# Optimization experiments

Measured on AMD Instinct MI355X. Metric: run time of the kernel, lower is better.

The kernel has to match this reference:

```python
import jax, jax.numpy as jnp
import numpy as np

B, T, C = 4, 4096, 512


def setup_inputs() -> dict:
    key = jax.random.key(0)
    ks = jax.random.split(key, 7)
    s = 1.0 / np.sqrt(C)  # ~ torch Linear init scale
    X = jax.random.normal(ks[0], (B, T, C), jnp.float32)
    S_n = jnp.zeros((B, C, C), jnp.float32)
    W_Q = jax.random.normal(ks[1], (C, C), jnp.float32) * s
    b_Q = jax.random.normal(ks[2], (C,), jnp.float32) * s
    W_K = jax.random.normal(ks[3], (C, C), jnp.float32) * s
    b_K = jax.random.normal(ks[4], (C,), jnp.float32) * s
    W_V = jax.random.normal(ks[5], (C, C), jnp.float32) * s
    b_V = jax.random.normal(ks[6], (C,), jnp.float32) * s
    return {"X": X, "S_n": S_n, "W_Q": W_Q, "b_Q": b_Q,
            "W_K": W_K, "b_K": b_K, "W_V": W_V, "b_V": b_V}


def reference(X, S_n, W_Q, b_Q, W_K, b_K, W_V, b_V):
    # forward_chunkwise with chunk_len = 1 (exact simplification):
    #   per step t (gamma g_t from linspace(0.96, 0.99, T)):
    #     inner_t = (q_t . k_t) * v_t            # D = gamma^0 = 1
    #     cross_t = (q_t @ S) * g_t              # e[:,0,:] = g^1
    #     O_t     = tanh(inner_t + cross_t)
    #     S      <- k_t^T v_t + g_t * S          # D[-1] = 1, g**chunk_len = g
    Bx, Tx, Cx = X.shape
    Q = X @ W_Q + b_Q  # [B,T,C]
    K = X @ W_K + b_K
    V = X @ W_V + b_V
    gammas = jnp.linspace(0.96, 0.99, Tx).astype(X.dtype)

    def step(S, inp):
        q, k, v, g = inp  # q,k,v: [B,C]; g: scalar
        inner = jnp.sum(q * k, axis=-1, keepdims=True) * v      # [B,C]
        cross = jnp.einsum('bc,bcd->bd', q, S) * g              # [B,C]
        O = jnp.tanh(inner + cross)
        S_new = jnp.einsum('bc,bd->bcd', k, v) + S * g          # [B,C,C]
        return S_new, O

    # original resets S_n to zeros regardless of the passed-in value
    S0 = jnp.zeros_like(S_n)
    S_final, O = jax.lax.scan(
        step, S0,
        (Q.transpose(1, 0, 2), K.transpose(1, 0, 2), V.transpose(1, 0, 2), gammas))
    out = O.transpose(1, 0, 2)  # [B,T,C]
    return out, S_final
```

## Files before the change

kernel.cpp:

```cpp
#include <hip/hip_runtime.h>
#include <math.h>

#define Bsz  4
#define Tlen 4096
#define Cdim 512
#define CUT  (-12.0f)
#define NBE  8388608

typedef unsigned int u32;
typedef _Float16 f16;
typedef __attribute__((ext_vector_type(8))) _Float16 f16x8;
typedef __attribute__((ext_vector_type(4))) float floatx4;
#define MFMA_F16(a,b,c) __builtin_amdgcn_mfma_f32_16x16x32_f16((a),(b),(c),0,0,0)

union pun8 { uint4 u; f16x8 f; };

__device__ __forceinline__ u32 pack2(f16 a, f16 b) {
    return (u32)__builtin_bit_cast(unsigned short, a) |
           ((u32)__builtin_bit_cast(unsigned short, b) << 16);
}
__device__ __forceinline__ u32 splitpack(float v) {
    f16 h = (f16)v;
    f16 l = (f16)(v - (float)h);
    return pack2(h, l);
}
__device__ __forceinline__ void unpack8(const u32* p, f16x8& h, f16x8& l) {
    uint4 q0 = *(const uint4*)p;
    uint4 q1 = *(const uint4*)(p + 4);
    pun8 ph, pl;
    ph.u.x = __builtin_amdgcn_perm(q0.y, q0.x, 0x05040100u);
    pl.u.x = __builtin_amdgcn_perm(q0.y, q0.x, 0x07060302u);
    ph.u.y = __builtin_amdgcn_perm(q0.w, q0.z, 0x05040100u);
    pl.u.y = __builtin_amdgcn_perm(q0.w, q0.z, 0x07060302u);
    ph.u.z = __builtin_amdgcn_perm(q1.y, q1.x, 0x05040100u);
    pl.u.z = __builtin_amdgcn_perm(q1.y, q1.x, 0x07060302u);
    ph.u.w = __builtin_amdgcn_perm(q1.w, q1.z, 0x05040100u);
    pl.u.w = __builtin_amdgcn_perm(q1.w, q1.z, 0x07060302u);
    h = ph.f; l = pl.f;
}
__device__ __forceinline__ float tanh_fast(float x) {
    return 1.0f - 2.0f / (__expf(2.0f * x) + 1.0f);
}

__global__ __launch_bounds__(256) void prep_kernel(
    const float* __restrict__ X,
    const float* __restrict__ WQ, const float* __restrict__ WK,
    const float* __restrict__ WV,
    f16* __restrict__ Xf, f16* __restrict__ WT,
    float* __restrict__ Lg, float* __restrict__ Wfin, int* __restrict__ sLo) {
    __shared__ char pshm[18432];
    int bid = blockIdx.x, tid = threadIdx.x;
    if (bid < 2048) {
        size_t i = ((size_t)bid * 256 + tid) * 16;
        float v[16];
#pragma unroll
        for (int j = 0; j < 4; ++j) {
            float4 a = *(const float4*)(X + i + j * 4);
            v[j*4+0]=a.x; v[j*4+1]=a.y; v[j*4+2]=a.z; v[j*4+3]=a.w;
        }
        uint4 o0, o1;
        o0.x = pack2((f16)v[0], (f16)v[1]);   o0.y = pack2((f16)v[2], (f16)v[3]);
        o0.z = pack2((f16)v[4], (f16)v[5]);   o0.w = pack2((f16)v[6], (f16)v[7]);
        o1.x = pack2((f16)v[8], (f16)v[9]);   o1.y = pack2((f16)v[10], (f16)v[11]);
        o1.z = pack2((f16)v[12], (f16)v[13]); o1.w = pack2((f16)v[14], (f16)v[15]);
        *(uint4*)(Xf + i) = o0;
        *(uint4*)(Xf + i + 8) = o1;
    } else if (bid < 2240) {
        f16* tile = (f16*)pshm;
        int wb = bid - 2048;
        int mat = wb >> 6, rem = wb & 63;
        int k0 = (rem >> 3) * 64, n0 = (rem & 7) * 64;
        const float* W = (mat == 0) ? WQ : (mat == 1) ? WK : WV;
        int row = tid >> 2, q = tid & 3;
        const float* src = W + (size_t)(k0 + row) * Cdim + n0 + q * 16;
        float vv[16];
#pragma unroll
        for (int j = 0; j < 4; ++j) {
            float4 v = *(const float4*)(src + j * 4);
            vv[j*4+0]=v.x; vv[j*4+1]=v.y; vv[j*4+2]=v.z; vv[j*4+3]=v.w;
        }
#pragma unroll
        for (int j = 0; j < 16; ++j) tile[(q * 16 + j) * 72 + row] = (f16)vv[j];
        __syncthreads();
        f16x8 r0 = *(const f16x8*)(tile + row * 72 + q * 16);
        f16x8 r1 = *(const f16x8*)(tile + row * 72 + q * 16 + 8);
        f16* dst = WT + ((size_t)mat * Cdim + n0 + row) * Cdim + k0 + q * 16;
        *(f16x8*)dst = r0;
        *(f16x8*)(dst + 8) = r1;
    } else {
        float* Lsh = (float*)pshm;
        float* sums = (float*)(pshm + 16400);
        float lg[16];
        float local = 0.f;
        int base = tid * 16;
#pragma unroll
        for (int i = 0; i < 16; ++i) {
            int t = base + i;
            float g = 0.96f + 0.03f * ((float)t * (1.0f / 4095.0f));
            lg[i] = logf(g);
            local += lg[i];
        }
        sums[tid] = local;
        __syncthreads();
        for (int off = 1; off < 256; off <<= 1) {
            float v = sums[tid];
            if (tid >= off) v += sums[tid - off];
            __syncthreads();
            sums[tid] = v;
            __syncthreads();
        }
        float pre = (tid == 0) ? 0.f : sums[tid - 1];
#pragma unroll
        for (int i = 0; i < 16; ++i) {
            Lsh[base + i] = pre;
            pre += lg[i];
        }
        if (tid == 255) Lsh[4096] = pre;
        __syncthreads();
        for (int t = tid; t < 4097; t += 256) Lg[t] = Lsh[t];
        float LT = Lsh[4096];
        for (int s = tid; s < 4096; s += 256) Wfin[s] = __expf(LT - Lsh[s + 1]);
        if (tid < 128) {
            float ref = Lsh[tid * 32 + 1];
            int st_hi = tid >> 2;
            int lo = st_hi;
            for (int st = 0; st < st_hi; ++st)
                if (ref - Lsh[st * 128 + 128] > CUT) { lo = st; break; }
            sLo[tid] = lo;
        }
    }
}

__global__ __launch_bounds__(256, 2) void qkv_mfma(
    const f16* __restrict__ Xf, const f16* __restrict__ WT,
    const float* __restrict__ bQ, const float* __restrict__ bK,
    const float* __restrict__ bV,
    f16* __restrict__ Qf, f16* __restrict__ Kf,
    f16* __restrict__ KT, f16* __restrict__ VT) {
    __shared__ char smem[34816];
    u32* sX = (u32*)smem;
    u32* sW = (u32*)(smem + 16384);
    f16* sB = (f16*)smem;

    int tid = threadIdx.x, lane = tid & 63, wid = tid >> 6;
    int l16 = lane & 15, quad = lane >> 4;
    int wm = wid & 1, wn = wid >> 1;
    int xb = blockIdx.x;
    int mat = xb >> 2, n0 = (xb & 3) * 128;
    int m0 = blockIdx.y * 128;

    floatx4 acc[4][4];
#pragma unroll
    for (int i = 0; i < 4; ++i)
#pragma unroll
        for (int j = 0; j < 4; ++j) acc[i][j] = (floatx4)0.f;

    int srow = tid >> 1, shalf = tid & 1;
    int arow_a = wm * 64 + l16, arow_b = wn * 64 + l16;
    int swz_f = (l16 & 7) << 2;

    for (int kc = 0; kc < Cdim; kc += 64) {
        __syncthreads();
        {
            const f16* gx = Xf + (size_t)(m0 + srow) * Cdim + kc + shalf * 32;
            const f16* gw = WT + ((size_t)(mat * Cdim) + n0 + srow) * Cdim + kc + shalf * 32;
            int wswz = (srow & 7) << 2;
#pragma unroll
            for (int k = 0; k < 4; ++k) {
                uint4 xv = *(const uint4*)(gx + k * 8);
                uint4 wv = *(const uint4*)(gw + k * 8);
                int w = shalf * 16 + k * 4;
                *(uint4*)&sX[srow * 32 + (w ^ wswz)] = xv;
                *(uint4*)&sW[srow * 32 + (w ^ wswz)] = wv;
            }
        }
        __syncthreads();
#pragma unroll
        for (int ks = 0; ks < 2; ++ks) {
            int w0 = ks * 16 + quad * 4;
            f16x8 af[4], bf[4];
#pragma unroll
            for (int mt = 0; mt < 4; ++mt)
                af[mt] = ((pun8*)&sX[(arow_a + mt * 16) * 32 + (w0 ^ swz_f)])->f;
#pragma unroll
            for (int nt = 0; nt < 4; ++nt)
                bf[nt] = ((pun8*)&sW[(arow_b + nt * 16) * 32 + (w0 ^ swz_f)])->f;
#pragma unroll
            for (int mt = 0; mt < 4; ++mt)
#pragma unroll
                for (int nt = 0; nt < 4; ++nt)
                    acc[mt][nt] = MFMA_F16(af[mt], bf[nt], acc[mt][nt]);
        }
    }

    const float* bias = (mat == 0) ? bQ : (mat == 1) ? bK : bV;
    float bv[4];
#pragma unroll
    for (int nt = 0; nt < 4; ++nt) bv[nt] = bias[n0 + wn * 64 + nt * 16 + l16];
    float cv[4][4][4];
#pragma unroll
    for (int mt = 0; mt < 4; ++mt)
#pragma unroll
        for (int nt = 0; nt < 4; ++nt)
#pragma unroll
            for (int r = 0; r < 4; ++r) cv[mt][nt][r] = acc[mt][nt][r] + bv[nt];

    int b = m0 >> 12, tloc = m0 & 4095;

    if (mat == 2) {
#pragma unroll
        for (int mt = 0; mt < 4; ++mt)
#pragma unroll
            for (int nt = 0; nt < 4; ++nt) {
                int d = n0 + wn * 64 + nt * 16 + l16;
                int t = tloc + wm * 64 + mt * 16 + quad * 4;
                uint2 w;
                w.x = pack2((f16)cv[mt][nt][0], (f16)cv[mt][nt][1]);
                w.y = pack2((f16)cv[mt][nt][2], (f16)cv[mt][nt][3]);
                *(uint2*)(VT + ((size_t)(b * Cdim + d)) * Tlen + t) = w;
            }
    } else {
        if (mat == 1) {
#pragma unroll
            for (int mt = 0; mt < 4; ++mt)
#pragma unroll
                for (int nt = 0; nt < 4; ++nt) {
                    int d = n0 + wn * 64 + nt * 16 + l16;
                    int t = tloc + wm * 64 + mt * 16 + quad * 4;
                    uint2 w;
                    w.x = pack2((f16)cv[mt][nt][0], (f16)cv[mt][nt][1]);
                    w.y = pack2((f16)cv[mt][nt][2], (f16)cv[mt][nt][3]);
                    *(uint2*)(KT + ((size_t)(b * Cdim + d)) * Tlen + t) = w;
                }
        }
        __syncthreads();
#pragma unroll
        for (int mt = 0; mt < 4; ++mt)
#pragma unroll
            for (int nt = 0; nt < 4; ++nt)
#pragma unroll
                for (int r = 0; r < 4; ++r)
                    sB[(wm * 64 + mt * 16 + quad * 4 + r) * 136 +
                       wn * 64 + nt * 16 + l16] = (f16)cv[mt][nt][r];
        __syncthreads();
        {
            f16* Out = (mat == 0) ? Qf : Kf;
            int r2 = tid >> 1, h2 = tid & 1;
            f16* dst = Out + (size_t)(m0 + r2) * Cdim + n0 + h2 * 64;
#pragma unroll
            for (int j = 0; j < 8; ++j)
                *(uint4*)(dst + j * 8) = *(const uint4*)(sB + r2 * 136 + h2 * 64 + j * 8);
        }
    }
}

__global__ __launch_bounds__(512, 4) void attn_mfma(
    const f16* __restrict__ Qf, const f16* __restrict__ Kf,
    const f16* __restrict__ VT, const f16* __restrict__ KT,
    const float* __restrict__ Lg, const float* __restrict__ Wfin,
    const int* __restrict__ sLo, float* __restrict__ out,
    float* __restrict__ S) {
    __shared__ char smem[66560];
    int tid = threadIdx.x, lane = tid & 63, wid = tid >> 6;
    int l16 = lane & 15, quad = lane >> 4;

    if (blockIdx.x >= 512) {
        f16* sA  = (f16*)smem;
        f16* sB2 = (f16*)(smem + 9216);
        int r = blockIdx.x - 512;
        int c0 = (r & 7) * 64, d0 = ((r >> 3) & 7) * 64, bb = r >> 6;
        int wv_c = wid & 3, wv_d = wid >> 2;
        float LT = Lg[Tlen];
        floatx4 acc[2];
        acc[0] = (floatx4)0.f; acc[1] = (floatx4)0.f;
        int s0start = Tlen - 64;
        for (int s0 = 0; s0 < Tlen; s0 += 64)
            if (LT - Lg[s0 + 64] > CUT) { s0start = s0; break; }
        int row = tid >> 3, q8 = (tid & 7) * 8;
        for (int s0 = s0start; s0 < Tlen; s0 += 64) {
            __syncthreads();
            {
                const f16* g = KT + ((size_t)(bb * Cdim + c0 + row)) * Tlen + s0 + q8;
                f16x8 u0 = *(const f16x8*)g;
                float4 w0 = *(const float4*)(Wfin + s0 + q8);
                float4 w1 = *(const float4*)(Wfin + s0 + q8 + 4);
                float wv[8] = {w0.x, w0.y, w0.z, w0.w, w1.x, w1.y, w1.z, w1.w};
                f16x8 o0;
#pragma unroll
                for (int j = 0; j < 8; ++j) o0[j] = (f16)((float)u0[j] * wv[j]);
                *(f16x8*)(sA + row * 72 + q8) = o0;
                const f16* gv = VT + ((size_t)(bb * Cdim + d0 + row)) * Tlen + s0 + q8;
                *(f16x8*)(sB2 + row * 72 + q8) = *(const f16x8*)gv;
            }
            __syncthreads();
#pragma unroll
            for (int ks = 0; ks < 2; ++ks) {
                int ko = ks * 32 + quad * 8;
                f16x8 a0 = *(const f16x8*)(sA + (wv_c * 16 + l16) * 72 + ko);
                f16x8 b0 = *(const f16x8*)(sB2 + (wv_d * 32 + l16) * 72 + ko);
                f16x8 b1 = *(const f16x8*)(sB2 + (wv_d * 32 + 16 + l16) * 72 + ko);
                acc[0] = MFMA_F16(a0, b0, acc[0]);
                acc[1] = MFMA_F16(a0, b1, acc[1]);
            }
        }
#pragma unroll
        for (int dt = 0; dt < 2; ++dt)
#pragma unroll
            for (int rr = 0; rr < 4; ++rr) {
                int c = c0 + wv_c * 16 + quad * 4 + rr;
                int d = d0 + wv_d * 32 + dt * 16 + l16;
                S[((size_t)(bb * Cdim + c)) * Cdim + d] = acc[dt][rr];
            }
        return;
    }

    u32* sQ  = (u32*)smem;
    u32* sPc = (u32*)(smem + 32768);

    int i = blockIdx.x;
    int halfsel = i >> 8, q = i & 255;
    int L = ((q & 7) << 5) | (q >> 3);
    int b = L >> 6, ttl = L & 63;
    int tt = halfsel ? (63 - ttl) : (64 + ttl);
    int t0 = tt * 32;
    size_t bT = (size_t)b * Tlen;
    int lo = sLo[tt], hi = tt >> 2;

    {
        int r = tid >> 4, c16 = tid & 15;
        const f16* src = Qf + (bT + t0 + r) * Cdim + c16 * 32;
        int wswz = (r & 7) << 2;
#pragma unroll
        for (int k = 0; k < 4; ++k) {
            uint4 v = *(const uint4*)(src + k * 8);
            int w = c16 * 16 + k * 4;
            *(uint4*)&sQ[r * 256 + (w ^ wswz)] = v;
        }
    }

    float aT[2][4];
#pragma unroll
    for (int mt = 0; mt < 2; ++mt)
#pragma unroll
        for (int r = 0; r < 4; ++r)
            aT[mt][r] = Lg[t0 + mt * 16 + quad * 4 + r + 1];

    floatx4 oacc[2][4];
#pragma unroll
    for (int mt = 0; mt < 2; ++mt)
#pragma unroll
        for (int nt = 0; nt < 4; ++nt) oacc[mt][nt] = (floatx4)0.f;

    int swz_f = (l16 & 7) << 2;
    int rowA0 = l16 * 256;
    int rowA1 = (16 + l16) * 256;

    __syncthreads();

    int pb = 0;
    for (int st = lo; st <= hi; ++st) {
        int s0 = st * 128;
        float lsp = Lg[s0 + wid * 16 + l16 + 1];

        floatx4 pacc[2];
        pacc[0] = (floatx4)0.f; pacc[1] = (floatx4)0.f;

        const f16* kb = Kf + (bT + s0 + wid * 16 + l16) * Cdim;
        const f16* vb = VT + ((size_t)(b * Cdim + wid * 64 + l16)) * Tlen + s0;

#pragma unroll 4
        for (int kc = 0; kc < 8; ++kc) {
            int ko = kc * 32 + quad * 8;
            int w0 = kc * 16 + quad * 4;
            f16x8 a0 = ((pun8*)&sQ[rowA0 + (w0 ^ swz_f)])->f;
            f16x8 a1 = ((pun8*)&sQ[rowA1 + (w0 ^ swz_f)])->f;
            f16x8 bk = *(const f16x8*)(kb + ko);
            pacc[0] = MFMA_F16(a0, bk, pacc[0]);
            pacc[1] = MFMA_F16(a1, bk, pacc[1]);
        }

        f16x8 vpre[2][4];
#pragma unroll
        for (int kf = 0; kf < 2; ++kf)
#pragma unroll
            for (int nt = 0; nt < 4; ++nt)
                vpre[kf][nt] = *(const f16x8*)(vb + (size_t)nt * 16 * Tlen +
                                               kf * 32 + quad * 8);

#pragma unroll 4
        for (int kc = 8; kc < 16; ++kc) {
            int ko = kc * 32 + quad * 8;
            int w0 = kc * 16 + quad * 4;
            f16x8 a0 = ((pun8*)&sQ[rowA0 + (w0 ^ swz_f)])->f;
            f16x8 a1 = ((pun8*)&sQ[rowA1 + (w0 ^ swz_f)])->f;
            f16x8 bk = *(const f16x8*)(kb + ko);
            pacc[0] = MFMA_F16(a0, bk, pacc[0]);
            pacc[1] = MFMA_F16(a1, bk, pacc[1]);
        }

        u32* sP = sPc + pb * 4224;
#pragma unroll
        for (int mt = 0; mt < 2; ++mt)
#pragma unroll
            for (int r = 0; r < 4; ++r) {
                int tl = mt * 16 + quad * 4 + r;
                int sl = wid * 16 + l16;
                int t = t0 + tl, s = s0 + sl;
                float p = pacc[mt][r];
                p = (s <= t) ? p * __expf(aT[mt][r] - lsp) : 0.f;
                sP[tl * 132 + (sl ^ ((tl & 7) << 4))] = splitpack(p);
            }
        __syncthreads();

        f16x8 vrest[2][4];
#pragma unroll
        for (int kf = 0; kf < 2; ++kf)
#pragma unroll
            for (int nt = 0; nt < 4; ++nt)
                vrest[kf][nt] = *(const f16x8*)(vb + (size_t)nt * 16 * Tlen +
                                                (kf + 2) * 32 + quad * 8);

#pragma unroll
        for (int kf = 0; kf < 4; ++kf) {
            int sb = kf * 32 + quad * 8;
            f16x8 ph[2], pl[2];
#pragma unroll
            for (int mt = 0; mt < 2; ++mt) {
                int tl = mt * 16 + l16;
                unpack8(&sP[tl * 132 + (sb ^ ((tl & 7) << 4))], ph[mt], pl[mt]);
            }
#pragma unroll
            for (int nt = 0; nt < 4; ++nt) {
                f16x8 vf = (kf < 2) ? vpre[kf][nt] : vrest[kf - 2][nt];
#pragma unroll
                for (int mt = 0; mt < 2; ++mt) {
                    oacc[mt][nt] = MFMA_F16(ph[mt], vf, oacc[mt][nt]);
                    oacc[mt][nt] = MFMA_F16(pl[mt], vf, oacc[mt][nt]);
                }
            }
        }
        pb ^= 1;
    }

#pragma unroll
    for (int mt = 0; mt < 2; ++mt)
#pragma unroll
        for (int nt = 0; nt < 4; ++nt)
#pragma unroll
            for (int r = 0; r < 4; ++r) {
                int t = t0 + mt * 16 + quad * 4 + r;
                int d = wid * 64 + nt * 16 + l16;
                out[(bT + t) * (size_t)Cdim + d] = tanh_fast(oacc[mt][nt][r]);
            }
}

extern "C" void kernel_launch(void* const* d_in, const int* in_sizes, int n_in,
                              void* d_out, int out_size, void* d_ws, size_t ws_size,
                              hipStream_t stream) {
    (void)in_sizes; (void)n_in; (void)out_size; (void)ws_size;
    const float* X  = (const float*)d_in[0];
    const float* WQ = (const float*)d_in[2];
    const float* bQ = (const float*)d_in[3];
    const float* WK = (const float*)d_in[4];
    const float* bK = (const float*)d_in[5];
    const float* WV = (const float*)d_in[6];
    const float* bV = (const float*)d_in[7];

    float* out   = (float*)d_out;
    float* S_out = out + (size_t)NBE;

    char* ws = (char*)d_ws;
    f16*   Xf   = (f16*)(ws);
    f16*   Qf   = (f16*)(ws + 2ull * NBE);
    f16*   Kf   = (f16*)(ws + 4ull * NBE);
    f16*   KT   = (f16*)(ws + 6ull * NBE);
    f16*   VT   = (f16*)(ws + 8ull * NBE);
    f16*   WT   = (f16*)(ws + 10ull * NBE);
    char*  tail = ws + 10ull * NBE + (2u << 20);
    float* Lg   = (float*)(tail);
    float* Wfin = (float*)(tail + 16512);
    int*   sLo  = (int*)(tail + 16512 + 16384);

    prep_kernel<<<2241, 256, 0, stream>>>(X, WQ, WK, WV, Xf, WT, Lg, Wfin, sLo);
    qkv_mfma<<<dim3(12, 128), 256, 0, stream>>>(Xf, WT, bQ, bK, bV, Qf, Kf, KT, VT);
    attn_mfma<<<768, 512, 0, stream>>>(Qf, Kf, VT, KT, Lg, Wfin, sLo, out, S_out);
}
```

Baseline: 266.2 us.

## Fuse X conversion into QKV GEMM, widen attention and state tiles

Drops the separate X-to-fp16 pass: the QKV GEMM now loads fp32 X and converts it while staging to shared memory. The attention kernel processes 256-key blocks instead of 128, with one shared P buffer in place of double buffering. The final-state blocks grow to 128x128 tiles, so fewer blocks are launched. The aim is less memory traffic and launch overhead and more reuse per block, at the cost of extra syncs, more registers, and direct global V loads in the second half of each block.

```diff
diff --git a/kernel.cpp b/kernel.cpp
--- a/kernel.cpp
+++ b/kernel.cpp
@@ -43,31 +43,15 @@
 }
 
 __global__ __launch_bounds__(256) void prep_kernel(
-    const float* __restrict__ X,
     const float* __restrict__ WQ, const float* __restrict__ WK,
     const float* __restrict__ WV,
-    f16* __restrict__ Xf, f16* __restrict__ WT,
+    f16* __restrict__ WT,
     float* __restrict__ Lg, float* __restrict__ Wfin, int* __restrict__ sLo) {
     __shared__ char pshm[18432];
     int bid = blockIdx.x, tid = threadIdx.x;
-    if (bid < 2048) {
-        size_t i = ((size_t)bid * 256 + tid) * 16;
-        float v[16];
-#pragma unroll
-        for (int j = 0; j < 4; ++j) {
-            float4 a = *(const float4*)(X + i + j * 4);
-            v[j*4+0]=a.x; v[j*4+1]=a.y; v[j*4+2]=a.z; v[j*4+3]=a.w;
-        }
-        uint4 o0, o1;
-        o0.x = pack2((f16)v[0], (f16)v[1]);   o0.y = pack2((f16)v[2], (f16)v[3]);
-        o0.z = pack2((f16)v[4], (f16)v[5]);   o0.w = pack2((f16)v[6], (f16)v[7]);
-        o1.x = pack2((f16)v[8], (f16)v[9]);   o1.y = pack2((f16)v[10], (f16)v[11]);
-        o1.z = pack2((f16)v[12], (f16)v[13]); o1.w = pack2((f16)v[14], (f16)v[15]);
-        *(uint4*)(Xf + i) = o0;
-        *(uint4*)(Xf + i + 8) = o1;
-    } else if (bid < 2240) {
+    if (bid < 192) {
         f16* tile = (f16*)pshm;
-        int wb = bid - 2048;
+        int wb = bid;
         int mat = wb >> 6, rem = wb & 63;
         int k0 = (rem >> 3) * 64, n0 = (rem & 7) * 64;
         const float* W = (mat == 0) ? WQ : (mat == 1) ? WK : WV;
@@ -122,17 +106,17 @@
         for (int s = tid; s < 4096; s += 256) Wfin[s] = __expf(LT - Lsh[s + 1]);
         if (tid < 128) {
             float ref = Lsh[tid * 32 + 1];
-            int st_hi = tid >> 2;
+            int st_hi = tid >> 3;
             int lo = st_hi;
             for (int st = 0; st < st_hi; ++st)
-                if (ref - Lsh[st * 128 + 128] > CUT) { lo = st; break; }
+                if (ref - Lsh[st * 256 + 256] > CUT) { lo = st; break; }
             sLo[tid] = lo;
         }
     }
 }
 
 __global__ __launch_bounds__(256, 2) void qkv_mfma(
-    const f16* __restrict__ Xf, const f16* __restrict__ WT,
+    const float* __restrict__ X, const f16* __restrict__ WT,
     const float* __restrict__ bQ, const float* __restrict__ bK,
     const float* __restrict__ bV,
     f16* __restrict__ Qf, f16* __restrict__ Kf,
@@ -162,12 +146,18 @@
     for (int kc = 0; kc < Cdim; kc += 64) {
         __syncthreads();
         {
-            const f16* gx = Xf + (size_t)(m0 + srow) * Cdim + kc + shalf * 32;
+            const float* gx = X + (size_t)(m0 + srow) * Cdim + kc + shalf * 32;
             const f16* gw = WT + ((size_t)(mat * Cdim) + n0 + srow) * Cdim + kc + shalf * 32;
             int wswz = (srow & 7) << 2;
 #pragma unroll
             for (int k = 0; k < 4; ++k) {
-                uint4 xv = *(const uint4*)(gx + k * 8);
+                float4 xa = *(const float4*)(gx + k * 8);
+                float4 xc = *(const float4*)(gx + k * 8 + 4);
+                uint4 xv;
+                xv.x = pack2((f16)xa.x, (f16)xa.y);
+                xv.y = pack2((f16)xa.z, (f16)xa.w);
+                xv.z = pack2((f16)xc.x, (f16)xc.y);
+                xv.w = pack2((f16)xc.z, (f16)xc.w);
                 uint4 wv = *(const uint4*)(gw + k * 8);
                 int w = shalf * 16 + k * 4;
                 *(uint4*)&sX[srow * 32 + (w ^ wswz)] = xv;
@@ -260,62 +250,83 @@
     const float* __restrict__ Lg, const float* __restrict__ Wfin,
     const int* __restrict__ sLo, float* __restrict__ out,
     float* __restrict__ S) {
-    __shared__ char smem[66560];
+    __shared__ char smem[66048];
     int tid = threadIdx.x, lane = tid & 63, wid = tid >> 6;
     int l16 = lane & 15, quad = lane >> 4;
 
     if (blockIdx.x >= 512) {
         f16* sA  = (f16*)smem;
-        f16* sB2 = (f16*)(smem + 9216);
+        f16* sB2 = (f16*)(smem + 18432);
         int r = blockIdx.x - 512;
-        int c0 = (r & 7) * 64, d0 = ((r >> 3) & 7) * 64, bb = r >> 6;
-        int wv_c = wid & 3, wv_d = wid >> 2;
+        int c0 = (r & 3) * 128, d0 = ((r >> 2) & 3) * 128, bb = r >> 4;
+        int wv_c = wid & 1, wv_d = wid >> 1;
         float LT = Lg[Tlen];
-        floatx4 acc[2];
-        acc[0] = (floatx4)0.f; acc[1] = (floatx4)0.f;
+        floatx4 acc[4][2];
+#pragma unroll
+        for (int i = 0; i < 4; ++i)
+#pragma unroll
+            for (int jj = 0; jj < 2; ++jj) acc[i][jj] = (floatx4)0.f;
         int s0start = Tlen - 64;
         for (int s0 = 0; s0 < Tlen; s0 += 64)
             if (LT - Lg[s0 + 64] > CUT) { s0start = s0; break; }
-        int row = tid >> 3, q8 = (tid & 7) * 8;
+        int row = tid >> 2, q16 = (tid & 3) * 16;
         for (int s0 = s0start; s0 < Tlen; s0 += 64) {
             __syncthreads();
             {
-                const f16* g = KT + ((size_t)(bb * Cdim + c0 + row)) * Tlen + s0 + q8;
+                const f16* g = KT + ((size_t)(bb * Cdim + c0 + row)) * Tlen + s0 + q16;
                 f16x8 u0 = *(const f16x8*)g;
-                float4 w0 = *(const float4*)(Wfin + s0 + q8);
-                float4 w1 = *(const float4*)(Wfin + s0 + q8 + 4);
-                float wv[8] = {w0.x, w0.y, w0.z, w0.w, w1.x, w1.y, w1.z, w1.w};
-                f16x8 o0;
-#pragma unroll
-                for (int j = 0; j < 8; ++j) o0[j] = (f16)((float)u0[j] * wv[j]);
-                *(f16x8*)(sA + row * 72 + q8) = o0;
-                const f16* gv = VT + ((size_t)(bb * Cdim + d0 + row)) * Tlen + s0 + q8;
-                *(f16x8*)(sB2 + row * 72 + q8) = *(const f16x8*)gv;
+                f16x8 u1 = *(const f16x8*)(g + 8);
+                float wv[16];
+#pragma unroll
+                for (int jj = 0; jj < 4; ++jj) {
+                    float4 w4 = *(const float4*)(Wfin + s0 + q16 + jj * 4);
+                    wv[jj*4+0]=w4.x; wv[jj*4+1]=w4.y; wv[jj*4+2]=w4.z; wv[jj*4+3]=w4.w;
+                }
+                f16x8 o0, o1;
+#pragma unroll
+                for (int jj = 0; jj < 8; ++jj) o0[jj] = (f16)((float)u0[jj] * wv[jj]);
+#pragma unroll
+                for (int jj = 0; jj < 8; ++jj) o1[jj] = (f16)((float)u1[jj] * wv[8 + jj]);
+                *(f16x8*)(sA + row * 72 + q16) = o0;
+                *(f16x8*)(sA + row * 72 + q16 + 8) = o1;
+                const f16* gv = VT + ((size_t)(bb * Cdim + d0 + row)) * Tlen + s0 + q16;
+                uint4 v0 = *(const uint4*)gv, v1 = *(const uint4*)(gv + 8);
+                *(uint4*)(sB2 + row * 72 + q16) = v0;
+                *(uint4*)(sB2 + row * 72 + q16 + 8) = v1;
             }
             __syncthreads();
 #pragma unroll
             for (int ks = 0; ks < 2; ++ks) {
                 int ko = ks * 32 + quad * 8;
-                f16x8 a0 = *(const f16x8*)(sA + (wv_c * 16 + l16) * 72 + ko);
-                f16x8 b0 = *(const f16x8*)(sB2 + (wv_d * 32 + l16) * 72 + ko);
-                f16x8 b1 = *(const f16x8*)(sB2 + (wv_d * 32 + 16 + l16) * 72 + ko);
-                acc[0] = MFMA_F16(a0, b0, acc[0]);
-                acc[1] = MFMA_F16(a0, b1, acc[1]);
-            }
-        }
-#pragma unroll
-        for (int dt = 0; dt < 2; ++dt)
-#pragma unroll
-            for (int rr = 0; rr < 4; ++rr) {
-                int c = c0 + wv_c * 16 + quad * 4 + rr;
-                int d = d0 + wv_d * 32 + dt * 16 + l16;
-                S[((size_t)(bb * Cdim + c)) * Cdim + d] = acc[dt][rr];
-            }
+                f16x8 av[4], bv2[2];
+#pragma unroll
+                for (int ct = 0; ct < 4; ++ct)
+                    av[ct] = *(const f16x8*)(sA + (wv_c * 64 + ct * 16 + l16) * 72 + ko);
+#pragma unroll
+                for (int dt = 0; dt < 2; ++dt)
+                    bv2[dt] = *(const f16x8*)(sB2 + (wv_d * 32 + dt * 16 + l16) * 72 + ko);
+#pragma unroll
+                for (int ct = 0; ct < 4; ++ct)
+#pragma unroll
+                    for (int dt = 0; dt < 2; ++dt)
+                        acc[ct][dt] = MFMA_F16(av[ct], bv2[dt], acc[ct][dt]);
+            }
+        }
+#pragma unroll
+        for (int ct = 0; ct < 4; ++ct)
+#pragma unroll
+            for (int dt = 0; dt < 2; ++dt)
+#pragma unroll
+                for (int rr = 0; rr < 4; ++rr) {
+                    int c = c0 + wv_c * 64 + ct * 16 + quad * 4 + rr;
+                    int d = d0 + wv_d * 32 + dt * 16 + l16;
+                    S[((size_t)(bb * Cdim + c)) * Cdim + d] = acc[ct][dt][rr];
+                }
         return;
     }
 
-    u32* sQ  = (u32*)smem;
-    u32* sPc = (u32*)(smem + 32768);
+    u32* sQ = (u32*)smem;
+    u32* sP = (u32*)(smem + 32768);
 
     int i = blockIdx.x;
     int halfsel = i >> 8, q = i & 255;
@@ -324,7 +335,7 @@
     int tt = halfsel ? (63 - ttl) : (64 + ttl);
     int t0 = tt * 32;
     size_t bT = (size_t)b * Tlen;
-    int lo = sLo[tt], hi = tt >> 2;
+    int lo = sLo[tt], hi = tt >> 3;
 
     {
         int r = tid >> 4, c16 = tid & 15;
@@ -357,15 +368,21 @@
 
     __syncthreads();
 
-    int pb = 0;
     for (int st = lo; st <= hi; ++st) {
-        int s0 = st * 128;
-        float lsp = Lg[s0 + wid * 16 + l16 + 1];
-
-        floatx4 pacc[2];
-        pacc[0] = (floatx4)0.f; pacc[1] = (floatx4)0.f;
-
-        const f16* kb = Kf + (bT + s0 + wid * 16 + l16) * Cdim;
+        int s0 = st * 256;
+        float lsp[2];
+#pragma unroll
+        for (int sq = 0; sq < 2; ++sq)
+            lsp[sq] = Lg[s0 + wid * 32 + sq * 16 + l16 + 1];
+
+        floatx4 pacc[2][2];
+#pragma unroll
+        for (int mt = 0; mt < 2; ++mt)
+#pragma unroll
+            for (int sq = 0; sq < 2; ++sq) pacc[mt][sq] = (floatx4)0.f;
+
+        const f16* kb0 = Kf + (bT + s0 + wid * 32 + l16) * Cdim;
+        const f16* kb1 = kb0 + 16 * Cdim;
         const f16* vb = VT + ((size_t)(b * Cdim + wid * 64 + l16)) * Tlen + s0;
 
 #pragma unroll 4
@@ -374,9 +391,12 @@
             int w0 = kc * 16 + quad * 4;
             f16x8 a0 = ((pun8*)&sQ[rowA0 + (w0 ^ swz_f)])->f;
             f16x8 a1 = ((pun8*)&sQ[rowA1 + (w0 ^ swz_f)])->f;
-            f16x8 bk = *(const f16x8*)(kb + ko);
-            pacc[0] = MFMA_F16(a0, bk, pacc[0]);
-            pacc[1] = MFMA_F16(a1, bk, pacc[1]);
+            f16x8 bk0 = *(const f16x8*)(kb0 + ko);
+            f16x8 bk1 = *(const f16x8*)(kb1 + ko);
+            pacc[0][0] = MFMA_F16(a0, bk0, pacc[0][0]);
+            pacc[0][1] = MFMA_F16(a0, bk1, pacc[0][1]);
+            pacc[1][0] = MFMA_F16(a1, bk0, pacc[1][0]);
+            pacc[1][1] = MFMA_F16(a1, bk1, pacc[1][1]);
         }
 
         f16x8 vpre[2][4];
@@ -393,23 +413,14 @@
             int w0 = kc * 16 + quad * 4;
             f16x8 a0 = ((pun8*)&sQ[rowA0 + (w0 ^ swz_f)])->f;
             f16x8 a1 = ((pun8*)&sQ[rowA1 + (w0 ^ swz_f)])->f;
-            f16x8 bk = *(const f16x8*)(kb + ko);
-            pacc[0] = MFMA_F16(a0, bk, pacc[0]);
-            pacc[1] = MFMA_F16(a1, bk, pacc[1]);
-        }
-
-        u32* sP = sPc + pb * 4224;
-#pragma unroll
-        for (int mt = 0; mt < 2; ++mt)
-#pragma unroll
-            for (int r = 0; r < 4; ++r) {
-                int tl = mt * 16 + quad * 4 + r;
-                int sl = wid * 16 + l16;
-                int t = t0 + tl, s = s0 + sl;
-                float p = pacc[mt][r];
-                p = (s <= t) ? p * __expf(aT[mt][r] - lsp) : 0.f;
-                sP[tl * 132 + (sl ^ ((tl & 7) << 4))] = splitpack(p);
-            }
+            f16x8 bk0 = *(const f16x8*)(kb0 + ko);
+            f16x8 bk1 = *(const f16x8*)(kb1 + ko);
+            pacc[0][0] = MFMA_F16(a0, bk0, pacc[0][0]);
+            pacc[0][1] = MFMA_F16(a0, bk1, pacc[0][1]);
+            pacc[1][0] = MFMA_F16(a1, bk0, pacc[1][0]);
+            pacc[1][1] = MFMA_F16(a1, bk1, pacc[1][1]);
+        }
+
         __syncthreads();
 
         f16x8 vrest[2][4];
@@ -421,17 +432,35 @@
                                                 (kf + 2) * 32 + quad * 8);
 
 #pragma unroll
-        for (int kf = 0; kf < 4; ++kf) {
+        for (int mt = 0; mt < 2; ++mt)
+#pragma unroll
+            for (int sq = 0; sq < 2; ++sq)
+#pragma unroll
+                for (int r = 0; r < 4; ++r) {
+                    int tl = mt * 16 + quad * 4 + r;
+                    int sl = wid * 32 + sq * 16 + l16;
+                    int t = t0 + tl, s = s0 + sl;
+                    float p = pacc[mt][sq][r];
+                    p = (s <= t) ? p * __expf(aT[mt][r] - lsp[sq]) : 0.f;
+                    sP[tl * 260 + (sl ^ ((tl & 7) << 4))] = splitpack(p);
+                }
+        __syncthreads();
+
+#pragma unroll
+        for (int kf = 0; kf < 8; ++kf) {
             int sb = kf * 32 + quad * 8;
             f16x8 ph[2], pl[2];
 #pragma unroll
             for (int mt = 0; mt < 2; ++mt) {
                 int tl = mt * 16 + l16;
-                unpack8(&sP[tl * 132 + (sb ^ ((tl & 7) << 4))], ph[mt], pl[mt]);
+                unpack8(&sP[tl * 260 + (sb ^ ((tl & 7) << 4))], ph[mt], pl[mt]);
             }
 #pragma unroll
             for (int nt = 0; nt < 4; ++nt) {
-                f16x8 vf = (kf < 2) ? vpre[kf][nt] : vrest[kf - 2][nt];
+                f16x8 vf;
+                if (kf < 2)      vf = vpre[kf][nt];
+                else if (kf < 4) vf = vrest[kf - 2][nt];
+                else             vf = *(const f16x8*)(vb + (size_t)nt * 16 * Tlen + sb);
 #pragma unroll
                 for (int mt = 0; mt < 2; ++mt) {
                     oacc[mt][nt] = MFMA_F16(ph[mt], vf, oacc[mt][nt]);
@@ -439,7 +468,6 @@
                 }
             }
         }
-        pb ^= 1;
     }
 
 #pragma unroll
@@ -470,18 +498,17 @@
     float* S_out = out + (size_t)NBE;
 
     char* ws = (char*)d_ws;
-    f16*   Xf   = (f16*)(ws);
-    f16*   Qf   = (f16*)(ws + 2ull * NBE);
-    f16*   Kf   = (f16*)(ws + 4ull * NBE);
-    f16*   KT   = (f16*)(ws + 6ull * NBE);
-    f16*   VT   = (f16*)(ws + 8ull * NBE);
-    f16*   WT   = (f16*)(ws + 10ull * NBE);
-    char*  tail = ws + 10ull * NBE + (2u << 20);
+    f16*   Qf   = (f16*)(ws);
+    f16*   Kf   = (f16*)(ws + 2ull * NBE);
+    f16*   KT   = (f16*)(ws + 4ull * NBE);
+    f16*   VT   = (f16*)(ws + 6ull * NBE);
+    f16*   WT   = (f16*)(ws + 8ull * NBE);
+    char*  tail = ws + 8ull * NBE + (2u << 20);
     float* Lg   = (float*)(tail);
     float* Wfin = (float*)(tail + 16512);
     int*   sLo  = (int*)(tail + 16512 + 16384);
 
-    prep_kernel<<<2241, 256, 0, stream>>>(X, WQ, WK, WV, Xf, WT, Lg, Wfin, sLo);
-    qkv_mfma<<<dim3(12, 128), 256, 0, stream>>>(Xf, WT, bQ, bK, bV, Qf, Kf, KT, VT);
-    attn_mfma<<<768, 512, 0, stream>>>(Qf, Kf, VT, KT, Lg, Wfin, sLo, out, S_out);
-}
+    prep_kernel<<<193, 256, 0, stream>>>(WQ, WK, WV, WT, Lg, Wfin, sLo);
+    qkv_mfma<<<dim3(12, 128), 256, 0, stream>>>(X, WT, bQ, bK, bV, Qf, Kf, KT, VT);
+    attn_mfma<<<576, 512, 0, stream>>>(Qf, Kf, VT, KT, Lg, Wfin, sLo, out, S_out);
+}
```

Result: slower. 323.9 us (+21.7%).
